# Optimization experiments

Hardware: AMD Instinct MI355X
Metric: run time of the kernel (lower is better)

The kernel has to match this reference:

```python
import jax, jax.numpy as jnp
import numpy as np

N_NODES = 100000
N_EDGES = 3200000
DIM = 64


def setup_inputs() -> dict:
    key = jax.random.key(0)
    k1, k2, k3, k4, k5, k6 = jax.random.split(key, 6)
    lap_rows = jax.random.randint(k1, (N_EDGES,), 0, N_NODES, dtype=jnp.int32)
    lap_cols = jax.random.randint(k2, (N_EDGES,), 0, N_NODES, dtype=jnp.int32)
    # normalized-Laplacian-like positive values
    lap_vals = jax.random.uniform(k3, (N_EDGES,), dtype=jnp.float32) * 0.1
    features = jax.random.normal(k4, (N_NODES, DIM), dtype=jnp.float32)
    scale = 1.0 / np.sqrt(DIM)
    W1 = jax.random.normal(k5, (DIM, DIM), dtype=jnp.float32) * scale
    b1 = jnp.zeros((DIM,), dtype=jnp.float32)
    W2 = jax.random.normal(k6, (DIM, DIM), dtype=jnp.float32) * scale
    b2 = jnp.zeros((DIM,), dtype=jnp.float32)
    return {
        "lap_rows": lap_rows, "lap_cols": lap_cols, "lap_vals": lap_vals,
        "features": features, "W1": W1, "b1": b1, "W2": W2, "b2": b2,
    }


def reference(lap_rows, lap_cols, lap_vals, features, W1, b1, W2, b2):
    # x = L @ features  (COO SpMM: gather source rows, scale, scatter-add to dest)
    msgs = lap_vals[:, None] * features[lap_cols]            # [E, D]
    x = jax.ops.segment_sum(msgs, lap_rows, num_segments=N_NODES)  # [N, D]
    # output = (L+I) E W1 + (L E * E) W2
    inter_part1 = (features + x) @ W1 + b1                   # [N, D_out]
    inter_part2 = (x * features) @ W2 + b2                   # [N, D_out]
    return inter_part1 + inter_part2
```

## Files before the change

kernel.cpp:

```cpp
#include <hip/hip_runtime.h>
#include <hip/hip_fp16.h>

#define DIM 64
#define RPB 64
#define RPB_SHIFT 6
#define SUP_SHIFT 11
#define SB_MAX 64
#define CAP 3072
#define CAPK (CAP / 1024)
#define HTILE_H 16384
#define HTILE1 8192
#define HTILE2 4096

typedef _Float16 half8 __attribute__((ext_vector_type(8)));
typedef float    f32x4 __attribute__((ext_vector_type(4)));
typedef float    f32x2 __attribute__((ext_vector_type(2)));

template <bool HI>
__device__ __forceinline__ __half2 q2h(unsigned int w)
{
    f32x2 f = __builtin_amdgcn_cvt_pk_f32_fp8(w, HI);
    return __floats2half2_rn(f[0], f[1]);
}

__global__ __launch_bounds__(256) void scatter_kernel(
    const int* __restrict__ rows, const int* __restrict__ cols,
    const float* __restrict__ vals, const float* __restrict__ feat,
    float* __restrict__ x, int E)
{
    unsigned long long t = (unsigned long long)blockIdx.x * blockDim.x + threadIdx.x;
    int e = (int)(t >> 6);
    int d = (int)(t & 63);
    if (e >= E) return;
    int r = rows[e];
    int c = cols[e];
    float v = vals[e];
    float f = feat[(size_t)c * DIM + d];
    atomicAdd(&x[(size_t)r * DIM + d], v * f);
}

__global__ __launch_bounds__(256) void cvt_kernel(
    const float* __restrict__ f, __half* __restrict__ h, int n2)
{
    int i = blockIdx.x * blockDim.x + threadIdx.x;
    if (i < n2) {
        float2 v = ((const float2*)f)[i];
        __half2 o;
        o.x = __float2half(v.x);
        o.y = __float2half(v.y);
        ((__half2*)h)[i] = o;
    }
}

__global__ __launch_bounds__(1024) void prep_kernel(
    const float* __restrict__ feat, __half* __restrict__ featH,
    unsigned char* __restrict__ featQ,
    const int* __restrict__ rows, int* __restrict__ gcnt,
    int n8, int NC, int E, int B)
{
    if ((int)blockIdx.x < NC) {
        int i = blockIdx.x * 1024 + threadIdx.x;
        if (i < n8) {
            const float4* src = (const float4*)(feat + (size_t)i * 8);
            float4 a = src[0], b = src[1];
            __half2 h0 = __floats2half2_rn(a.x, a.y);
            __half2 h1 = __floats2half2_rn(a.z, a.w);
            __half2 h2 = __floats2half2_rn(b.x, b.y);
            __half2 h3 = __floats2half2_rn(b.z, b.w);
            float4 ho;
            ho.x = __builtin_bit_cast(float, h0);
            ho.y = __builtin_bit_cast(float, h1);
            ho.z = __builtin_bit_cast(float, h2);
            ho.w = __builtin_bit_cast(float, h3);
            *(float4*)(featH + (size_t)i * 8) = ho;
            unsigned int q0 = __builtin_amdgcn_cvt_pk_fp8_f32(a.x, a.y, 0, false);
            q0 = __builtin_amdgcn_cvt_pk_fp8_f32(a.z, a.w, (int)q0, true);
            unsigned int q1 = __builtin_amdgcn_cvt_pk_fp8_f32(b.x, b.y, 0, false);
            q1 = __builtin_amdgcn_cvt_pk_fp8_f32(b.z, b.w, (int)q1, true);
            uint2 qo; qo.x = q0; qo.y = q1;
            *(uint2*)(featQ + (size_t)i * 8) = qo;
        }
    } else {
        extern __shared__ int lcnt[];
        for (int i = threadIdx.x; i < B; i += 1024) lcnt[i] = 0;
        __syncthreads();
        int base = ((int)blockIdx.x - NC) * HTILE_H;
#pragma unroll
        for (int k = 0; k < HTILE_H / 1024; ++k) {
            int e = base + k * 1024 + threadIdx.x;
            if (e < E) atomicAdd(&lcnt[rows[e] >> RPB_SHIFT], 1);
        }
        __syncthreads();
        for (int i = threadIdx.x; i < B; i += 1024)
            if (lcnt[i]) atomicAdd(&gcnt[i], lcnt[i]);
    }
}

__global__ __launch_bounds__(1024) void scan_kernel(
    const int* __restrict__ gcnt, int* __restrict__ offs, int* __restrict__ cursors,
    int* __restrict__ soffs, int* __restrict__ scursors, int B, int SB, int E)
{
    __shared__ int lds[2048];
    int t = threadIdx.x;
    int c0 = (t < B) ? gcnt[t] : 0;
    int c1 = (t + 1024 < B) ? gcnt[t + 1024] : 0;
    lds[t] = c0;
    lds[t + 1024] = c1;
    __syncthreads();
    for (int off = 1; off < 2048; off <<= 1) {
        int a = (t >= off) ? lds[t - off] : 0;
        int b = lds[t + 1024 - off];
        __syncthreads();
        lds[t] += a;
        lds[t + 1024] += b;
        __syncthreads();
    }
    if (t < B) {
        int e = lds[t] - c0;
        offs[t] = e; cursors[t] = e;
        if ((t & 31) == 0) { soffs[t >> 5] = e; scursors[t >> 5] = e; }
    }
    int t2 = t + 1024;
    if (t2 < B) {
        int e = lds[t2] - c1;
        offs[t2] = e; cursors[t2] = e;
        if ((t2 & 31) == 0) { soffs[t2 >> 5] = e; scursors[t2 >> 5] = e; }
    }
    if (t == 0) { offs[B] = E; soffs[SB] = E; }
}

__global__ __launch_bounds__(1024) void superbin_kernel(
    const int* __restrict__ rows, const int* __restrict__ cols,
    const float* __restrict__ vals, int* __restrict__ scursors,
    unsigned long long* __restrict__ sorted1, int E, int SB)
{
    __shared__ int cnt[SB_MAX];
    __shared__ int bse[SB_MAX];
    const int tid = threadIdx.x;
    if (tid < SB) cnt[tid] = 0;
    __syncthreads();
    const int tbase = blockIdx.x * HTILE1;
    int rr[HTILE1 / 1024];
#pragma unroll
    for (int k = 0; k < HTILE1 / 1024; ++k) {
        int e = tbase + k * 1024 + tid;
        rr[k] = (e < E) ? rows[e] : -1;
        if (rr[k] >= 0) atomicAdd(&cnt[rr[k] >> SUP_SHIFT], 1);
    }
    __syncthreads();
    if (tid < SB) {
        int c = cnt[tid];
        bse[tid] = c ? atomicAdd(&scursors[tid], c) : 0;
        cnt[tid] = 0;
    }
    __syncthreads();
#pragma unroll
    for (int k = 0; k < HTILE1 / 1024; ++k) {
        int e = tbase + k * 1024 + tid;
        if (rr[k] >= 0) {
            int r  = rr[k];
            int sb = r >> SUP_SHIFT;
            int slot = bse[sb] + atomicAdd(&cnt[sb], 1);
            unsigned long long pk =
                ((unsigned long long)__float_as_uint(vals[e]) << 32) |
                ((unsigned long long)(r & 2047) << 17) |
                (unsigned)cols[e];
            sorted1[slot] = pk;
        }
    }
}

__global__ __launch_bounds__(1024) void finebin_kernel(
    const unsigned long long* __restrict__ sorted1, const int* __restrict__ soffs,
    int* __restrict__ cursors, unsigned long long* __restrict__ sorted2,
    int E, int B, int SB)
{
    extern __shared__ int l[];
    int* cnt  = l;
    int* bse  = l + B;
    int* sofl = l + 2 * B;
    const int tid = threadIdx.x;
    if (tid <= SB) sofl[tid] = soffs[tid];
    for (int i = tid; i < B; i += 1024) cnt[i] = 0;
    __syncthreads();

    const int tbase = blockIdx.x * HTILE2;
    int sb0 = 0;
    {
        int lo = 0, hi = SB - 1;
        while (lo < hi) {
            int mid = (lo + hi + 1) >> 1;
            if (sofl[mid] <= tbase) lo = mid; else hi = mid - 1;
        }
        sb0 = lo;
    }

    unsigned long long pkr[HTILE2 / 1024];
    int fidr[HTILE2 / 1024];
#pragma unroll
    for (int k = 0; k < HTILE2 / 1024; ++k) {
        int i = tbase + k * 1024 + tid;
        if (i < E) {
            pkr[k] = sorted1[i];
            int sb = sb0;
            while (sofl[sb + 1] <= i) sb++;
            fidr[k] = (sb << 5) + (int)((pkr[k] >> 23) & 31);
            atomicAdd(&cnt[fidr[k]], 1);
        } else fidr[k] = -1;
    }
    __syncthreads();
    for (int i = tid; i < B; i += 1024) {
        int c = cnt[i];
        bse[i] = c ? atomicAdd(&cursors[i], c) : 0;
    }
    __syncthreads();
    for (int i = tid; i < B; i += 1024) cnt[i] = 0;
    __syncthreads();
#pragma unroll
    for (int k = 0; k < HTILE2 / 1024; ++k) {
        if (fidr[k] >= 0) {
            int f = fidr[k];
            int slot = bse[f] + atomicAdd(&cnt[f], 1);
            sorted2[slot] = pkr[k];
        }
    }
}

__global__ __launch_bounds__(1024, 8) void reduce_fused_mfma_kernel(
    const unsigned long long* __restrict__ sorted, const int* __restrict__ offs,
    const unsigned char* __restrict__ featQ, const __half* __restrict__ featH,
    const float* __restrict__ W1, const float* __restrict__ b1,
    const float* __restrict__ W2, const float* __restrict__ b2,
    float* __restrict__ out, int N)
{
    __shared__ unsigned long long spk[CAP];
    __shared__ int rcnt[RPB];
    __shared__ int rbase[RPB];
    __shared__ float xs[RPB][DIM + 4];
    __shared__ half8 Wl[1024];
    __shared__ float biasl[DIM];

    const int tid = threadIdx.x;
    const int b   = blockIdx.x;
    const int w    = tid >> 6;
    const int lane = tid & 63;

    {
        int t    = tid >> 8;
        int c    = (tid >> 6) & 3;
        int quad = (tid >> 4) & 3;
        int m    = tid & 15;
        const float* Wsrc = (t < 2) ? W1 : W2;
        int kbase = (t & 1) * 32 + quad * 8;
        int col   = c * 16 + m;
        half8 wv;
#pragma unroll
        for (int j = 0; j < 8; ++j)
            wv[j] = (_Float16)Wsrc[(kbase + j) * DIM + col];
        Wl[tid] = wv;
        if (tid < DIM) biasl[tid] = b1[tid] + b2[tid];
    }

    const int s    = offs[b];
    const int tend = offs[b + 1];
    int nl = tend - s;
    if (nl > CAP) nl = CAP;

    if (tid < RPB) rcnt[tid] = 0;
    __syncthreads();

    unsigned long long pkreg[CAPK];
#pragma unroll
    for (int k = 0; k < CAPK; ++k) {
        int i = k * 1024 + tid;
        pkreg[k] = (i < nl) ? __builtin_nontemporal_load(sorted + s + i) : 0ull;
    }
#pragma unroll
    for (int k = 0; k < CAPK; ++k) {
        int i = k * 1024 + tid;
        if (i < nl) atomicAdd(&rcnt[(int)((pkreg[k] >> 17) & (RPB - 1))], 1);
    }
    __syncthreads();

    if (tid < 64) {
        int c = rcnt[tid];
        int v = c;
#pragma unroll
        for (int off = 1; off < 64; off <<= 1) {
            int u = __shfl_up(v, off, 64);
            if (tid >= off) v += u;
        }
        rbase[tid] = v - c;
        rcnt[tid]  = 0;
    }
    __syncthreads();

#pragma unroll
    for (int k = 0; k < CAPK; ++k) {
        int i = k * 1024 + tid;
        if (i < nl) {
            int rl  = (int)((pkreg[k] >> 17) & (RPB - 1));
            int idx = atomicAdd(&rcnt[rl], 1);
            spk[rbase[rl] + idx] = pkreg[k];
        }
    }
    __syncthreads();

    const int eg   = lane >> 3;
    const int sub  = lane & 7;
    const int rowbase = b * RPB;

#define GATHER(PK) (*(const uint2*)(featQ + ((size_t)((PK) & 0x1FFFFu) << 6) + sub * 8))

    {
        const int rl = 4 * w + (eg >> 1);
        const int g  = eg & 1;
        const int rs = rbase[rl];
        const int rt = rs + rcnt[rl];

        int cg = rt - (rs + g);
        cg = (cg > 0) ? ((cg + 1) >> 1) : 0;
        int kmax = (cg + 1) >> 1;
#pragma unroll
        for (int off = 1; off < 64; off <<= 1) {
            int u = __shfl_xor(kmax, off, 64);
            kmax = (u > kmax) ? u : kmax;
        }

        __half2 hacc[4];
#pragma unroll
        for (int q = 0; q < 4; ++q) hacc[q] = __floats2half2_rn(0.f, 0.f);

        int idx = rs + g;
        for (int k = 0; k < kmax; ++k, idx += 4) {
            bool p0 = idx < rt;
            bool p1 = idx + 2 < rt;
            unsigned long long pk0 = p0 ? spk[idx] : 0ull;
            unsigned long long pk1 = p1 ? spk[idx + 2] : 0ull;
            uint2 q0 = GATHER(pk0);
            uint2 q1 = GATHER(pk1);
            __half2 v0 = __float2half2_rn(__uint_as_float((unsigned)(pk0 >> 32)));
            __half2 v1 = __float2half2_rn(__uint_as_float((unsigned)(pk1 >> 32)));
            hacc[0] = __hfma2(v0, q2h<false>(q0.x), hacc[0]);
            hacc[1] = __hfma2(v0, q2h<true >(q0.x), hacc[1]);
            hacc[2] = __hfma2(v0, q2h<false>(q0.y), hacc[2]);
            hacc[3] = __hfma2(v0, q2h<true >(q0.y), hacc[3]);
            hacc[0] = __hfma2(v1, q2h<false>(q1.x), hacc[0]);
            hacc[1] = __hfma2(v1, q2h<true >(q1.x), hacc[1]);
            hacc[2] = __hfma2(v1, q2h<false>(q1.y), hacc[2]);
            hacc[3] = __hfma2(v1, q2h<true >(q1.y), hacc[3]);
        }

        float acc[8];
#pragma unroll
        for (int q = 0; q < 4; ++q) {
            acc[2 * q]     = __low2float(hacc[q]);
            acc[2 * q + 1] = __high2float(hacc[q]);
        }
#pragma unroll
        for (int q = 0; q < 8; ++q)
            acc[q] += __shfl_xor(acc[q], 8, 64);

        if (g == 0) {
            float4 o0; o0.x = acc[0]; o0.y = acc[1]; o0.z = acc[2]; o0.w = acc[3];
            float4 o1; o1.x = acc[4]; o1.y = acc[5]; o1.z = acc[6]; o1.w = acc[7];
            *(float4*)&xs[rl][sub * 8]     = o0;
            *(float4*)&xs[rl][sub * 8 + 4] = o1;
        }
    }
#undef GATHER
    __syncthreads();

    if (tend - s > CAP) {
        for (int e = s + CAP + tid; e < tend; e += 1024) {
            unsigned long long pk = sorted[e];
            int rl = (int)((pk >> 17) & (RPB - 1));
            float v = __uint_as_float((unsigned)(pk >> 32));
            int c = (int)(pk & 0x1FFFFu);
            for (int d = 0; d < DIM; ++d)
                atomicAdd(&xs[rl][d], v * __half2float(featH[(size_t)c * DIM + d]));
        }
        __syncthreads();
    }

    {
        const int m    = lane & 15;
        const int quad = lane >> 4;
        const int tile = w >> 2;
        const int cw   = w & 3;

        const int fb = cw * 64 + quad * 16 + m;
        half8 wf0 = Wl[fb];
        half8 wf1 = Wl[fb + 256];
        half8 wf2 = Wl[fb + 512];
        half8 wf3 = Wl[fb + 768];
        float bias = biasl[cw * 16 + m];

        int rowl = tile * 16 + m;
        int grow = rowbase + rowl;
        int rldr = (grow < N) ? grow : (N - 1);
        const __half* fp = featH + (size_t)rldr * DIM + quad * 8;
        half8 flo = *(const half8*)(fp);
        half8 fhi = *(const half8*)(fp + 32);
        const float* xp = &xs[rowl][quad * 8];
        float4 xl0 = *(const float4*)(xp);
        float4 xl1 = *(const float4*)(xp + 4);
        float4 xh0 = *(const float4*)(xp + 32);
        float4 xh1 = *(const float4*)(xp + 36);

        half8 alo, ahi, blo, bhi;
        _Float16 xv;
        xv = (_Float16)xl0.x; alo[0] = flo[0] + xv; blo[0] = flo[0] * xv;
        xv = (_Float16)xl0.y; alo[1] = flo[1] + xv; blo[1] = flo[1] * xv;
        xv = (_Float16)xl0.z; alo[2] = flo[2] + xv; blo[2] = flo[2] * xv;
        xv = (_Float16)xl0.w; alo[3] = flo[3] + xv; blo[3] = flo[3] * xv;
        xv = (_Float16)xl1.x; alo[4] = flo[4] + xv; blo[4] = flo[4] * xv;
        xv = (_Float16)xl1.y; alo[5] = flo[5] + xv; blo[5] = flo[5] * xv;
        xv = (_Float16)xl1.z; alo[6] = flo[6] + xv; blo[6] = flo[6] * xv;
        xv = (_Float16)xl1.w; alo[7] = flo[7] + xv; blo[7] = flo[7] * xv;
        xv = (_Float16)xh0.x; ahi[0] = fhi[0] + xv; bhi[0] = fhi[0] * xv;
        xv = (_Float16)xh0.y; ahi[1] = fhi[1] + xv; bhi[1] = fhi[1] * xv;
        xv = (_Float16)xh0.z; ahi[2] = fhi[2] + xv; bhi[2] = fhi[2] * xv;
        xv = (_Float16)xh0.w; ahi[3] = fhi[3] + xv; bhi[3] = fhi[3] * xv;
        xv = (_Float16)xh1.x; ahi[4] = fhi[4] + xv; bhi[4] = fhi[4] * xv;
        xv = (_Float16)xh1.y; ahi[5] = fhi[5] + xv; bhi[5] = fhi[5] * xv;
        xv = (_Float16)xh1.z; ahi[6] = fhi[6] + xv; bhi[6] = fhi[6] * xv;
        xv = (_Float16)xh1.w; ahi[7] = fhi[7] + xv; bhi[7] = fhi[7] * xv;

        f32x4 a0 = { bias, bias, bias, bias };
        a0 = __builtin_amdgcn_mfma_f32_16x16x32_f16(alo, wf0, a0, 0, 0, 0);
        a0 = __builtin_amdgcn_mfma_f32_16x16x32_f16(ahi, wf1, a0, 0, 0, 0);
        a0 = __builtin_amdgcn_mfma_f32_16x16x32_f16(blo, wf2, a0, 0, 0, 0);
        a0 = __builtin_amdgcn_mfma_f32_16x16x32_f16(bhi, wf3, a0, 0, 0, 0);

#pragma unroll
        for (int reg = 0; reg < 4; ++reg) {
            int orow = rowbase + tile * 16 + quad * 4 + reg;
            if (orow < N)
                out[(size_t)orow * DIM + cw * 16 + m] = a0[reg];
        }
    }
}

__global__ __launch_bounds__(256) void transform_mfma_kernel(
    const __half* __restrict__ featH, const float* __restrict__ x,
    const float* __restrict__ W1, const float* __restrict__ b1,
    const float* __restrict__ W2, const float* __restrict__ b2,
    float* __restrict__ out, int N)
{
    const int lane = threadIdx.x & 63;
    const int m    = lane & 15;
    const int quad = lane >> 4;

    half8 wfrag[4][4];
#pragma unroll
    for (int t = 0; t < 4; ++t) {
        const float* Wsrc = (t < 2) ? W1 : W2;
        int kbase = (t & 1) * 32 + quad * 8;
#pragma unroll
        for (int c = 0; c < 4; ++c) {
            int col = c * 16 + m;
            half8 w;
#pragma unroll
            for (int j = 0; j < 8; ++j)
                w[j] = (_Float16)Wsrc[(kbase + j) * DIM + col];
            wfrag[t][c] = w;
        }
    }
    float bias[4];
#pragma unroll
    for (int c = 0; c < 4; ++c)
        bias[c] = b1[c * 16 + m] + b2[c * 16 + m];

    const int ntiles = (N + 15) / 16;
    const int wid    = (int)((blockIdx.x * blockDim.x + threadIdx.x) >> 6);
    const int nwaves = (int)((gridDim.x * blockDim.x) >> 6);

    for (int tile = wid; tile < ntiles; tile += nwaves) {
        int row  = tile * 16 + m;
        int rldr = (row < N) ? row : (N - 1);
        const __half* fp = featH + (size_t)rldr * DIM + quad * 8;
        const float*  xp = x     + (size_t)rldr * DIM + quad * 8;
        half8 flo = *(const half8*)(fp);
        half8 fhi = *(const half8*)(fp + 32);
        float4 xl0 = *(const float4*)(xp);
        float4 xl1 = *(const float4*)(xp + 4);
        float4 xh0 = *(const float4*)(xp + 32);
        float4 xh1 = *(const float4*)(xp + 36);

        half8 alo, ahi, blo, bhi;
        _Float16 xv;
        xv = (_Float16)xl0.x; alo[0] = flo[0] + xv; blo[0] = flo[0] * xv;
        xv = (_Float16)xl0.y; alo[1] = flo[1] + xv; blo[1] = flo[1] * xv;
        xv = (_Float16)xl0.z; alo[2] = flo[2] + xv; blo[2] = flo[2] * xv;
        xv = (_Float16)xl0.w; alo[3] = flo[3] + xv; blo[3] = flo[3] * xv;
        xv = (_Float16)xl1.x; alo[4] = flo[4] + xv; blo[4] = flo[4] * xv;
        xv = (_Float16)xl1.y; alo[5] = flo[5] + xv; blo[5] = flo[5] * xv;
        xv = (_Float16)xl1.z; alo[6] = flo[6] + xv; blo[6] = flo[6] * xv;
        xv = (_Float16)xl1.w; alo[7] = flo[7] + xv; blo[7] = flo[7] * xv;
        xv = (_Float16)xh0.x; ahi[0] = fhi[0] + xv; bhi[0] = fhi[0] * xv;
        xv = (_Float16)xh0.y; ahi[1] = fhi[1] + xv; bhi[1] = fhi[1] * xv;
        xv = (_Float16)xh0.z; ahi[2] = fhi[2] + xv; bhi[2] = fhi[2] * xv;
        xv = (_Float16)xh0.w; ahi[3] = fhi[3] + xv; bhi[3] = fhi[3] * xv;
        xv = (_Float16)xh1.x; ahi[4] = fhi[4] + xv; bhi[4] = fhi[4] * xv;
        xv = (_Float16)xh1.y; ahi[5] = fhi[5] + xv; bhi[5] = fhi[5] * xv;
        xv = (_Float16)xh1.z; ahi[6] = fhi[6] + xv; bhi[6] = fhi[6] * xv;
        xv = (_Float16)xh1.w; ahi[7] = fhi[7] + xv; bhi[7] = fhi[7] * xv;

        f32x4 acc[4];
#pragma unroll
        for (int c = 0; c < 4; ++c) {
            f32x4 a0 = { bias[c], bias[c], bias[c], bias[c] };
            a0 = __builtin_amdgcn_mfma_f32_16x16x32_f16(alo, wfrag[0][c], a0, 0, 0, 0);
            a0 = __builtin_amdgcn_mfma_f32_16x16x32_f16(ahi, wfrag[1][c], a0, 0, 0, 0);
            a0 = __builtin_amdgcn_mfma_f32_16x16x32_f16(blo, wfrag[2][c], a0, 0, 0, 0);
            a0 = __builtin_amdgcn_mfma_f32_16x16x32_f16(bhi, wfrag[3][c], a0, 0, 0, 0);
            acc[c] = a0;
        }

#pragma unroll
        for (int reg = 0; reg < 4; ++reg) {
            int orow = tile * 16 + quad * 4 + reg;
            if (orow < N) {
#pragma unroll
                for (int c = 0; c < 4; ++c)
                    out[(size_t)orow * DIM + c * 16 + m] = acc[c][reg];
            }
        }
    }
}

extern "C" void kernel_launch(void* const* d_in, const int* in_sizes, int n_in,
                              void* d_out, int out_size, void* d_ws, size_t ws_size,
                              hipStream_t stream)
{
    const int*   rows = (const int*)d_in[0];
    const int*   cols = (const int*)d_in[1];
    const float* vals = (const float*)d_in[2];
    const float* feat = (const float*)d_in[3];
    const float* W1   = (const float*)d_in[4];
    const float* b1   = (const float*)d_in[5];
    const float* W2   = (const float*)d_in[6];
    const float* b2   = (const float*)d_in[7];
    float* out = (float*)d_out;

    const int E  = in_sizes[0];
    const int N  = in_sizes[3] / DIM;
    const int B  = (N + RPB - 1) / RPB;
    const int SB = (B + 31) / 32;

    char* ws = (char*)d_ws;
    size_t xBytes     = (size_t)N * DIM * sizeof(float);
    size_t hBytes     = (((size_t)N * DIM * sizeof(__half)) + 255) / 256 * 256;
    size_t qBytes     = (((size_t)N * DIM) + 255) / 256 * 256;
    size_t offsBytes  = (((size_t)(B + 1) * sizeof(int)) + 255) / 256 * 256;
    size_t cursBytes  = (((size_t)B * sizeof(int)) + 255) / 256 * 256;
    size_t soffBytes  = (((size_t)(SB + 1) * sizeof(int)) + 255) / 256 * 256;
    size_t scurBytes  = (((size_t)SB * sizeof(int)) + 255) / 256 * 256;
    size_t sortBytes  = (size_t)E * 8;

    float*              x        = (float*)ws;
    __half*             featH    = (__half*)(ws + xBytes);
    unsigned char*      featQ    = (unsigned char*)(ws + xBytes + hBytes);
    int*                offs     = (int*)(ws + xBytes + hBytes + qBytes);
    int*                cursors  = (int*)(ws + xBytes + hBytes + qBytes + offsBytes);
    int*                soffs    = (int*)(ws + xBytes + hBytes + qBytes + offsBytes + cursBytes);
    int*                scursors = (int*)(ws + xBytes + hBytes + qBytes + offsBytes + cursBytes + soffBytes);
    unsigned long long* sorted1  = (unsigned long long*)(ws + xBytes + hBytes + qBytes + offsBytes +
                                                         cursBytes + soffBytes + scurBytes);
    unsigned long long* sorted2  = sorted1 + E;
    size_t need = xBytes + hBytes + qBytes + offsBytes + cursBytes + soffBytes + scurBytes + 2 * sortBytes;

    if (ws_size >= need && B <= 2048 && SB <= SB_MAX && N <= 131072) {
        const int n8  = N * DIM / 8;
        const int NC  = (n8 + 1023) / 1024;
        const int NTH = (E + HTILE_H - 1) / HTILE_H;
        const int NT1 = (E + HTILE1 - 1) / HTILE1;
        const int NT2 = (E + HTILE2 - 1) / HTILE2;
        hipMemsetAsync(offs, 0, (size_t)(B + 1) * sizeof(int), stream);
        prep_kernel<<<NC + NTH, 1024, (size_t)B * 4, stream>>>(
            feat, featH, featQ, rows, offs, n8, NC, E, B);
        scan_kernel<<<1, 1024, 0, stream>>>(offs, offs, cursors, soffs, scursors, B, SB, E);
        superbin_kernel<<<NT1, 1024, 0, stream>>>(rows, cols, vals, scursors, sorted1, E, SB);
        finebin_kernel<<<NT2, 1024, (size_t)(2 * B + SB + 1) * 4, stream>>>(
            sorted1, soffs, cursors, sorted2, E, B, SB);
        reduce_fused_mfma_kernel<<<B, 1024, 0, stream>>>(sorted2, offs, featQ, featH,
                                                         W1, b1, W2, b2, out, N);
    } else {
        cvt_kernel<<<(N * DIM / 2 + 255) / 256, 256, 0, stream>>>(feat, featH, N * DIM / 2);
        hipMemsetAsync(x, 0, xBytes, stream);
        unsigned long long threads = (unsigned long long)E * DIM;
        unsigned int blocks = (unsigned int)((threads + 255ull) / 256ull);
        scatter_kernel<<<blocks, 256, 0, stream>>>(rows, cols, vals, feat, x, E);
        transform_mfma_kernel<<<640, 256, 0, stream>>>(featH, x, W1, b1, W2, b2, out, N);
    }
}
```

Before: 228.3 us.

## Stage binned edges in LDS for coalesced writes in superbin and finebin passes

Both binning passes now compute a local prefix over bin counts, place the packed edges into a shared-memory staging buffer grouped by bin, then copy each bin out contiguously. The goal is to replace scattered 8-byte global stores with coalesced runs. Finebin also drops its B-sized dynamic LDS arrays in favour of a 256-entry local window of fine bins starting at the tile's first superbin, falling back to per-element global atomics when a tile spans more than that window. Tile sizes are halved to fit the staging buffers, which doubles the number of blocks and the number of global cursor atomics.

```diff
diff --git a/kernel.cpp b/kernel.cpp
--- a/kernel.cpp
+++ b/kernel.cpp
@@ -9,8 +9,9 @@
 #define CAP 3072
 #define CAPK (CAP / 1024)
 #define HTILE_H 16384
-#define HTILE1 8192
-#define HTILE2 4096
+#define HTILE1 4096
+#define HTILE2 2048
+#define FB_LOC 256
 
 typedef _Float16 half8 __attribute__((ext_vector_type(8)));
 typedef float    f32x4 __attribute__((ext_vector_type(4)));
@@ -134,10 +135,12 @@
     const float* __restrict__ vals, int* __restrict__ scursors,
     unsigned long long* __restrict__ sorted1, int E, int SB)
 {
+    __shared__ unsigned long long stg[HTILE1];
     __shared__ int cnt[SB_MAX];
-    __shared__ int bse[SB_MAX];
+    __shared__ int lbase[SB_MAX];
+    __shared__ int gbase[SB_MAX];
     const int tid = threadIdx.x;
-    if (tid < SB) cnt[tid] = 0;
+    if (tid < SB_MAX) cnt[tid] = 0;
     __syncthreads();
     const int tbase = blockIdx.x * HTILE1;
     int rr[HTILE1 / 1024];
@@ -148,9 +151,16 @@
         if (rr[k] >= 0) atomicAdd(&cnt[rr[k] >> SUP_SHIFT], 1);
     }
     __syncthreads();
-    if (tid < SB) {
+    if (tid < 64) {
         int c = cnt[tid];
-        bse[tid] = c ? atomicAdd(&scursors[tid], c) : 0;
+        int v = c;
+#pragma unroll
+        for (int off = 1; off < 64; off <<= 1) {
+            int u = __shfl_up(v, off, 64);
+            if (tid >= off) v += u;
+        }
+        lbase[tid] = v - c;
+        gbase[tid] = (c > 0 && tid < SB) ? atomicAdd(&scursors[tid], c) : 0;
         cnt[tid] = 0;
     }
     __syncthreads();
@@ -160,13 +170,22 @@
         if (rr[k] >= 0) {
             int r  = rr[k];
             int sb = r >> SUP_SHIFT;
-            int slot = bse[sb] + atomicAdd(&cnt[sb], 1);
+            int idx = atomicAdd(&cnt[sb], 1);
             unsigned long long pk =
                 ((unsigned long long)__float_as_uint(vals[e]) << 32) |
                 ((unsigned long long)(r & 2047) << 17) |
                 (unsigned)cols[e];
-            sorted1[slot] = pk;
-        }
+            stg[lbase[sb] + idx] = pk;
+        }
+    }
+    __syncthreads();
+    const int wv = tid >> 6, ln = tid & 63;
+    for (int sb = wv; sb < SB; sb += 16) {
+        int n  = cnt[sb];
+        int lb = lbase[sb];
+        int gb = gbase[sb];
+        for (int i = ln; i < n; i += 64)
+            sorted1[gb + i] = stg[lb + i];
     }
 }
 
@@ -175,13 +194,16 @@
     int* __restrict__ cursors, unsigned long long* __restrict__ sorted2,
     int E, int B, int SB)
 {
-    extern __shared__ int l[];
-    int* cnt  = l;
-    int* bse  = l + B;
-    int* sofl = l + 2 * B;
+    __shared__ unsigned long long stg[HTILE2];
+    __shared__ int cnt[FB_LOC];
+    __shared__ int lbase[FB_LOC];
+    __shared__ int gbase[FB_LOC];
+    __shared__ int sofl[SB_MAX + 1];
+    __shared__ int spanbad;
     const int tid = threadIdx.x;
     if (tid <= SB) sofl[tid] = soffs[tid];
-    for (int i = tid; i < B; i += 1024) cnt[i] = 0;
+    if (tid < FB_LOC) cnt[tid] = 0;
+    if (tid == 0) spanbad = 0;
     __syncthreads();
 
     const int tbase = blockIdx.x * HTILE2;
@@ -194,9 +216,10 @@
         }
         sb0 = lo;
     }
+    const int fid0 = sb0 << 5;
 
     unsigned long long pkr[HTILE2 / 1024];
-    int fidr[HTILE2 / 1024];
+    int fl[HTILE2 / 1024];
 #pragma unroll
     for (int k = 0; k < HTILE2 / 1024; ++k) {
         int i = tbase + k * 1024 + tid;
@@ -204,25 +227,61 @@
             pkr[k] = sorted1[i];
             int sb = sb0;
             while (sofl[sb + 1] <= i) sb++;
-            fidr[k] = (sb << 5) + (int)((pkr[k] >> 23) & 31);
-            atomicAdd(&cnt[fidr[k]], 1);
-        } else fidr[k] = -1;
-    }
-    __syncthreads();
-    for (int i = tid; i < B; i += 1024) {
-        int c = cnt[i];
-        bse[i] = c ? atomicAdd(&cursors[i], c) : 0;
-    }
-    __syncthreads();
-    for (int i = tid; i < B; i += 1024) cnt[i] = 0;
+            int l = ((sb - sb0) << 5) + (int)((pkr[k] >> 23) & 31);
+            fl[k] = l;
+            if (l >= FB_LOC) spanbad = 1;
+            else atomicAdd(&cnt[l], 1);
+        } else fl[k] = -1;
+    }
+    __syncthreads();
+
+    if (spanbad) {
+#pragma unroll
+        for (int k = 0; k < HTILE2 / 1024; ++k) {
+            if (fl[k] >= 0) {
+                int fidg = fid0 + fl[k];
+                int slot = atomicAdd(&cursors[fidg], 1);
+                sorted2[slot] = pkr[k];
+            }
+        }
+        return;
+    }
+
+    if (tid < 64) {
+        int carry = 0;
+#pragma unroll
+        for (int ch = 0; ch < FB_LOC / 64; ++ch) {
+            int idx = ch * 64 + tid;
+            int c = cnt[idx];
+            int v = c;
+#pragma unroll
+            for (int off = 1; off < 64; off <<= 1) {
+                int u = __shfl_up(v, off, 64);
+                if (tid >= off) v += u;
+            }
+            lbase[idx] = carry + v - c;
+            int gfid = fid0 + idx;
+            gbase[idx] = (c > 0 && gfid < B) ? atomicAdd(&cursors[gfid], c) : 0;
+            cnt[idx] = 0;
+            carry += __shfl(v, 63, 64);
+        }
+    }
     __syncthreads();
 #pragma unroll
     for (int k = 0; k < HTILE2 / 1024; ++k) {
-        if (fidr[k] >= 0) {
-            int f = fidr[k];
-            int slot = bse[f] + atomicAdd(&cnt[f], 1);
-            sorted2[slot] = pkr[k];
-        }
+        if (fl[k] >= 0) {
+            int idx = atomicAdd(&cnt[fl[k]], 1);
+            stg[lbase[fl[k]] + idx] = pkr[k];
+        }
+    }
+    __syncthreads();
+    const int wv = tid >> 6, ln = tid & 63;
+    for (int f = wv; f < FB_LOC; f += 16) {
+        int n = cnt[f];
+        if (!n) continue;
+        int lb = lbase[f], gb = gbase[f];
+        for (int i = ln; i < n; i += 64)
+            sorted2[gb + i] = stg[lb + i];
     }
 }
 
@@ -318,9 +377,9 @@
         const int rs = rbase[rl];
         const int rt = rs + rcnt[rl];
 
-        int cg = rt - (rs + g);
-        cg = (cg > 0) ? ((cg + 1) >> 1) : 0;
-        int kmax = (cg + 1) >> 1;
+        int cg2 = rt - (rs + g);
+        cg2 = (cg2 > 0) ? ((cg2 + 1) >> 1) : 0;
+        int kmax = (cg2 + 1) >> 1;
 #pragma unroll
         for (int off = 1; off < 64; off <<= 1) {
             int u = __shfl_xor(kmax, off, 64);
@@ -577,18 +636,17 @@
         const int NTH = (E + HTILE_H - 1) / HTILE_H;
         const int NT1 = (E + HTILE1 - 1) / HTILE1;
         const int NT2 = (E + HTILE2 - 1) / HTILE2;
-        hipMemsetAsync(offs, 0, (size_t)(B + 1) * sizeof(int), stream);
+        (void)hipMemsetAsync(offs, 0, (size_t)(B + 1) * sizeof(int), stream);
         prep_kernel<<<NC + NTH, 1024, (size_t)B * 4, stream>>>(
             feat, featH, featQ, rows, offs, n8, NC, E, B);
         scan_kernel<<<1, 1024, 0, stream>>>(offs, offs, cursors, soffs, scursors, B, SB, E);
         superbin_kernel<<<NT1, 1024, 0, stream>>>(rows, cols, vals, scursors, sorted1, E, SB);
-        finebin_kernel<<<NT2, 1024, (size_t)(2 * B + SB + 1) * 4, stream>>>(
-            sorted1, soffs, cursors, sorted2, E, B, SB);
+        finebin_kernel<<<NT2, 1024, 0, stream>>>(sorted1, soffs, cursors, sorted2, E, B, SB);
         reduce_fused_mfma_kernel<<<B, 1024, 0, stream>>>(sorted2, offs, featQ, featH,
                                                          W1, b1, W2, b2, out, N);
     } else {
         cvt_kernel<<<(N * DIM / 2 + 255) / 256, 256, 0, stream>>>(feat, featH, N * DIM / 2);
-        hipMemsetAsync(x, 0, xBytes, stream);
+        (void)hipMemsetAsync(x, 0, xBytes, stream);
         unsigned long long threads = (unsigned long long)E * DIM;
         unsigned int blocks = (unsigned int)((threads + 255ull) / 256ull);
         scatter_kernel<<<blocks, 256, 0, stream>>>(rows, cols, vals, feat, x, E);
```

Result: no change. 224.4 us (-1.7%).
